# Kernel optimization log

Hardware: AMD Instinct MI355X
Metric: run time of the kernel (lower is better)

The kernel has to match this reference:

```python
import jax, jax.numpy as jnp
import numpy as np

NEG_SLOPE = 0.2
EPS = 1e-16


def _gat_conv(x_src, x_dst, src, dst, W_src, W_dst, a_src, a_dst, b):
    """Single-head bipartite GAT-style conv (gather-score-softmax-scatter)."""
    num_dst = x_dst.shape[0]
    h_src = x_src @ W_src                      # [Ns, C]
    h_dst = x_dst @ W_dst                      # [Nd, C]
    s_src = h_src @ a_src                      # [Ns]
    s_dst = h_dst @ a_dst                      # [Nd]
    e = jax.nn.leaky_relu(s_src[src] + s_dst[dst], NEG_SLOPE)  # [E]
    # segment softmax over incoming edges of each dst node
    m = jax.ops.segment_max(e, dst, num_segments=num_dst)      # [Nd]
    w = jnp.exp(e - m[dst])
    denom = jax.ops.segment_sum(w, dst, num_segments=num_dst)  # [Nd]
    alpha = w / (denom[dst] + EPS)                             # [E]
    out = jax.ops.segment_sum(alpha[:, None] * h_src[src], dst, num_segments=num_dst)
    return out + b


def setup_inputs() -> dict:
    key = jax.random.key(0)
    ks = jax.random.split(key, 32)
    N_a, N_p, N_v = 100000, 150000, 10000
    F_in, C = 768, 64
    E_w, E_c, E_p = 300000, 1500000, 150000
    sc_in = 1.0 / np.sqrt(F_in)
    sc_c = 1.0 / np.sqrt(C)
    inp = {
        'x_author': jax.random.normal(ks[0], (N_a, F_in), jnp.float32),
        'x_paper': jax.random.normal(ks[1], (N_p, F_in), jnp.float32),
        'x_venue': jax.random.normal(ks[2], (N_v, F_in), jnp.float32),
        'writes_src': jax.random.randint(ks[3], (E_w,), 0, N_a, jnp.int32),
        'writes_dst': jax.random.randint(ks[4], (E_w,), 0, N_p, jnp.int32),
        'cites_src': jax.random.randint(ks[5], (E_c,), 0, N_p, jnp.int32),
        'cites_dst': jax.random.randint(ks[6], (E_c,), 0, N_p, jnp.int32),
        'pub_src': jax.random.randint(ks[7], (E_p,), 0, N_v, jnp.int32),
        'pub_dst': jax.random.randint(ks[8], (E_p,), 0, N_p, jnp.int32),
    }
    # per-edge-type learned params: W_src, W_dst [F_in, C], att vecs [C], bias [C]
    names = ['w', 'c', 'p']  # writes, cites, publishes
    for i, n in enumerate(names):
        base = 9 + 5 * i
        inp[f'W{n}_src'] = jax.random.normal(ks[base + 0], (F_in, C), jnp.float32) * sc_in
        inp[f'W{n}_dst'] = jax.random.normal(ks[base + 1], (F_in, C), jnp.float32) * sc_in
        inp[f'a{n}_src'] = jax.random.normal(ks[base + 2], (C,), jnp.float32) * sc_c
        inp[f'a{n}_dst'] = jax.random.normal(ks[base + 3], (C,), jnp.float32) * sc_c
        inp[f'b{n}'] = jnp.zeros((C,), jnp.float32)
    return inp


def reference(x_author, x_paper, x_venue,
              writes_src, writes_dst, cites_src, cites_dst, pub_src, pub_dst,
              Ww_src, Ww_dst, aw_src, aw_dst, bw,
              Wc_src, Wc_dst, ac_src, ac_dst, bc,
              Wp_src, Wp_dst, ap_src, ap_dst, bp):
    # HeteroConv with aggr='sum': all three edge types target 'paper'
    out_w = _gat_conv(x_author, x_paper, writes_src, writes_dst, Ww_src, Ww_dst, aw_src, aw_dst, bw)
    out_c = _gat_conv(x_paper, x_paper, cites_src, cites_dst, Wc_src, Wc_dst, ac_src, ac_dst, bc)
    out_p = _gat_conv(x_venue, x_paper, pub_src, pub_dst, Wp_src, Wp_dst, ap_src, ap_dst, bp)
    return out_w + out_c + out_p  # [N_paper, out_channels]
```

## Files before the change

### kernel.cpp

```cpp
#include <hip/hip_runtime.h>


#define F_IN 768
#define C_OUT 64
#define BN 80
#define TILE_M 64
#define BK 64
#define LDK 72
#define EPS 1e-16f

typedef __bf16 bf16x8 __attribute__((ext_vector_type(8)));
typedef float  f32x4  __attribute__((ext_vector_type(4)));

__global__ void prep_weights(
    const float* __restrict__ Ww_src, const float* __restrict__ aw_src,
    const float* __restrict__ Wc_src, const float* __restrict__ ac_src,
    const float* __restrict__ Wp_src, const float* __restrict__ ap_src,
    const float* __restrict__ Ww_dst, const float* __restrict__ aw_dst,
    const float* __restrict__ Wc_dst, const float* __restrict__ ac_dst,
    const float* __restrict__ Wp_dst, const float* __restrict__ ap_dst,
    __bf16* __restrict__ WTw, __bf16* __restrict__ WTc, __bf16* __restrict__ WTp)
{
    int type = blockIdx.x;
    const float* Ws = (type == 0) ? Ww_src : (type == 1) ? Wc_src : Wp_src;
    const float* as = (type == 0) ? aw_src : (type == 1) ? ac_src : ap_src;
    __bf16* WT = (type == 0) ? WTw : (type == 1) ? WTc : WTp;

    for (int r = threadIdx.x; r < F_IN; r += blockDim.x) {
        const float* wrow = Ws + (size_t)r * C_OUT;
        float u = 0.f;
        for (int c = 0; c < C_OUT; ++c) {
            float wv = wrow[c];
            WT[(size_t)c * F_IN + r] = (__bf16)wv;
            u += wv * as[c];
        }
        WT[(size_t)64 * F_IN + r] = (__bf16)u;
        for (int c = 65; c < BN; ++c) WT[(size_t)c * F_IN + r] = (__bf16)0.f;
        if (type == 1) {
            const float* r1 = Ww_dst + (size_t)r * C_OUT;
            const float* r2 = Wc_dst + (size_t)r * C_OUT;
            const float* r3 = Wp_dst + (size_t)r * C_OUT;
            float vw = 0.f, vc = 0.f, vp = 0.f;
            for (int c = 0; c < C_OUT; ++c) {
                vw += r1[c] * aw_dst[c];
                vc += r2[c] * ac_dst[c];
                vp += r3[c] * ap_dst[c];
            }
            WT[(size_t)65 * F_IN + r] = (__bf16)vw;
            WT[(size_t)66 * F_IN + r] = (__bf16)vc;
            WT[(size_t)67 * F_IN + r] = (__bf16)vp;
        }
    }
}

__global__ __launch_bounds__(256) void gemm_fused(
    const float* __restrict__ X, const __bf16* __restrict__ WT,
    float* __restrict__ H,
    float* __restrict__ s0, float* __restrict__ s1,
    float* __restrict__ s2, float* __restrict__ s3, int M)
{
    __shared__ __bf16 As[TILE_M][LDK];
    __shared__ __bf16 Bs[BN][LDK];

    const int tid  = threadIdx.x;
    const int lane = tid & 63;
    const int warp = tid >> 6;
    const int colq = lane & 15;
    const int quad = lane >> 4;
    const int rowBase = blockIdx.x * TILE_M;

    f32x4 acc[5];
#pragma unroll
    for (int t = 0; t < 5; ++t) acc[t] = (f32x4){0.f, 0.f, 0.f, 0.f};

    const int arow  = tid >> 2;
    const int akoff = (tid & 3) * 16;
    const int grow  = rowBase + arow;
    const bool rowOK = grow < M;
    const float* xrow = X + (size_t)grow * F_IN;

    for (int kc = 0; kc < F_IN; kc += BK) {
        f32x4 av[4];
        if (rowOK) {
            const f32x4* xp = (const f32x4*)(xrow + kc + akoff);
            av[0] = xp[0]; av[1] = xp[1]; av[2] = xp[2]; av[3] = xp[3];
        } else {
#pragma unroll
            for (int i = 0; i < 4; ++i) av[i] = (f32x4){0.f, 0.f, 0.f, 0.f};
        }
        bf16x8 cv[2];
#pragma unroll
        for (int i = 0; i < 4; ++i)
#pragma unroll
            for (int j = 0; j < 4; ++j)
                cv[i >> 1][(i & 1) * 4 + j] = (__bf16)av[i][j];
        *(bf16x8*)&As[arow][akoff]     = cv[0];
        *(bf16x8*)&As[arow][akoff + 8] = cv[1];

        for (int c = tid; c < (BN * BK / 8); c += 256) {
            int br = c >> 3, bo = (c & 7) * 8;
            *(bf16x8*)&Bs[br][bo] =
                *(const bf16x8*)&WT[(size_t)br * F_IN + kc + bo];
        }
        __syncthreads();

#pragma unroll
        for (int kk = 0; kk < BK; kk += 32) {
            bf16x8 a = *(const bf16x8*)&As[warp * 16 + colq][kk + quad * 8];
#pragma unroll
            for (int t = 0; t < 5; ++t) {
                bf16x8 b = *(const bf16x8*)&Bs[t * 16 + colq][kk + quad * 8];
                acc[t] = __builtin_amdgcn_mfma_f32_16x16x32_bf16(a, b, acc[t], 0, 0, 0);
            }
        }
        __syncthreads();
    }

    const int orow0 = rowBase + warp * 16 + quad * 4;
#pragma unroll
    for (int r = 0; r < 4; ++r) {
        int row = orow0 + r;
        if (row < M) {
#pragma unroll
            for (int t = 0; t < 4; ++t)
                H[(size_t)row * C_OUT + t * 16 + colq] = acc[t][r];
            if (colq < 4) {
                float* sp = (colq == 0) ? s0 : (colq == 1) ? s1 : (colq == 2) ? s2 : s3;
                if (sp) sp[row] = acc[4][r];
            }
        }
    }
}

__global__ void hist3(const int* __restrict__ d1, int E1,
                      const int* __restrict__ d2, int E2,
                      const int* __restrict__ d3, int E3,
                      int* __restrict__ cnt)
{
    int i0 = blockIdx.x * blockDim.x + threadIdx.x;
    int stride = gridDim.x * blockDim.x;
    for (int i = i0; i < E1; i += stride) atomicAdd(&cnt[d1[i]], 1);
    for (int i = i0; i < E2; i += stride) atomicAdd(&cnt[d2[i]], 1);
    for (int i = i0; i < E3; i += stride) atomicAdd(&cnt[d3[i]], 1);
}

__global__ void scan1(const int* __restrict__ cnt, int n,
                      int* __restrict__ rowptr, int* __restrict__ bsums)
{
    __shared__ int sm[256];
    const int t = threadIdx.x;
    const int base = blockIdx.x * 1024 + t * 4;
    int v[4];
    int tot = 0;
#pragma unroll
    for (int k = 0; k < 4; ++k) {
        v[k] = (base + k < n) ? cnt[base + k] : 0;
        tot += v[k];
    }
    sm[t] = tot;
    __syncthreads();
    for (int off = 1; off < 256; off <<= 1) {
        int add = (t >= off) ? sm[t - off] : 0;
        __syncthreads();
        sm[t] += add;
        __syncthreads();
    }
    int run = sm[t] - tot;
#pragma unroll
    for (int k = 0; k < 4; ++k) {
        if (base + k < n) rowptr[base + k] = run;
        run += v[k];
    }
    if (t == 255) bsums[blockIdx.x] = sm[255];
}

__global__ void scan2(int* __restrict__ bsums, int nb)
{
    __shared__ int sm[256];
    const int t = threadIdx.x;
    int v = (t < nb) ? bsums[t] : 0;
    sm[t] = v;
    __syncthreads();
    for (int off = 1; off < 256; off <<= 1) {
        int add = (t >= off) ? sm[t - off] : 0;
        __syncthreads();
        sm[t] += add;
        __syncthreads();
    }
    if (t < nb) bsums[t] = sm[t] - v;
}

__global__ void scan3(const int* __restrict__ bsums, int n, int Etot,
                      int* __restrict__ rowptr, int* __restrict__ cursor)
{
    int i = blockIdx.x * blockDim.x + threadIdx.x;
    if (i < n) {
        int r = rowptr[i] + bsums[i >> 10];
        rowptr[i] = r;
        cursor[i] = r;
    }
    if (i == 0) rowptr[n] = Etot;
}

__global__ void edge_sort3(const int* __restrict__ s1, const int* __restrict__ d1, int E1,
                           const int* __restrict__ s2, const int* __restrict__ d2, int E2,
                           const int* __restrict__ s3, const int* __restrict__ d3, int E3,
                           int* __restrict__ cursor, unsigned* __restrict__ eidx)
{
    int i0 = blockIdx.x * blockDim.x + threadIdx.x;
    int stride = gridDim.x * blockDim.x;
    for (int i = i0; i < E1; i += stride) {
        int p = atomicAdd(&cursor[d1[i]], 1);
        eidx[p] = (0u << 24) | (unsigned)s1[i];
    }
    for (int i = i0; i < E2; i += stride) {
        int p = atomicAdd(&cursor[d2[i]], 1);
        eidx[p] = (1u << 24) | (unsigned)s2[i];
    }
    for (int i = i0; i < E3; i += stride) {
        int p = atomicAdd(&cursor[d3[i]], 1);
        eidx[p] = (2u << 24) | (unsigned)s3[i];
    }
}

__global__ __launch_bounds__(256) void gat_gather(
    const unsigned* __restrict__ eidx, const int* __restrict__ rowptr,
    const float* __restrict__ Ha, const float* __restrict__ Hp, const float* __restrict__ Hv,
    const float* __restrict__ ssw, const float* __restrict__ ssc, const float* __restrict__ ssp,
    const float* __restrict__ sdw, const float* __restrict__ sdc, const float* __restrict__ sdp,
    const float* __restrict__ bw, const float* __restrict__ bc, const float* __restrict__ bp,
    float* __restrict__ out, int Nd)
{
    const int lane = threadIdx.x & 63;
    const int q    = lane & 15;
    const int gbase = lane & ~15;
    const int gid  = (blockIdx.x * blockDim.x + threadIdx.x) >> 4;
    const int ng   = (gridDim.x * blockDim.x) >> 4;

    const f32x4* Ha4 = (const f32x4*)Ha;
    const f32x4* Hp4 = (const f32x4*)Hp;
    const f32x4* Hv4 = (const f32x4*)Hv;
    f32x4* out4 = (f32x4*)out;

    const f32x4 b4 = ((const f32x4*)bw)[q] + ((const f32x4*)bc)[q] + ((const f32x4*)bp)[q];

    for (int d = gid; d < Nd; d += ng) {
        const int start = rowptr[d];
        const int end   = rowptr[d + 1];
        const float sd0 = sdw[d], sd1 = sdc[d], sd2 = sdp[d];
        f32x4 a0 = (f32x4){0.f,0.f,0.f,0.f};
        f32x4 a1 = (f32x4){0.f,0.f,0.f,0.f};
        f32x4 a2 = (f32x4){0.f,0.f,0.f,0.f};
        float dn0 = 0.f, dn1 = 0.f, dn2 = 0.f;

        for (int base = start; base < end; base += 16) {
            int n = end - base;
            if (n > 16) n = 16;
            unsigned ew = 0u;
            float w = 0.f;
            if (q < n) {
                ew = eidx[base + q];
                int t = (int)(ew >> 24);
                int s = (int)(ew & 0xFFFFFFu);
                float ss = (t == 0) ? ssw[s] : (t == 1) ? ssc[s] : ssp[s];
                float sd = (t == 0) ? sd0 : (t == 1) ? sd1 : sd2;
                float e = ss + sd;
                e = (e >= 0.f) ? e : 0.2f * e;
                w = __expf(e);
                if (t == 0) dn0 += w; else if (t == 1) dn1 += w; else dn2 += w;
            }
            int j = 0;
            for (; j + 2 <= n; j += 2) {
#pragma unroll
                for (int u = 0; u < 2; ++u) {
                    float wj = __shfl(w, gbase + j + u);
                    unsigned ej = (unsigned)__shfl((int)ew, gbase + j + u);
                    int tj = (int)(ej >> 24);
                    int sj = (int)(ej & 0xFFFFFFu);
                    const f32x4* Hr = (tj == 0) ? Ha4 : (tj == 1) ? Hp4 : Hv4;
                    f32x4 hv = Hr[(size_t)sj * 16 + q];
                    if (tj == 0) a0 += wj * hv;
                    else if (tj == 1) a1 += wj * hv;
                    else a2 += wj * hv;
                }
            }
            for (; j < n; ++j) {
                float wj = __shfl(w, gbase + j);
                unsigned ej = (unsigned)__shfl((int)ew, gbase + j);
                int tj = (int)(ej >> 24);
                int sj = (int)(ej & 0xFFFFFFu);
                const f32x4* Hr = (tj == 0) ? Ha4 : (tj == 1) ? Hp4 : Hv4;
                f32x4 hv = Hr[(size_t)sj * 16 + q];
                if (tj == 0) a0 += wj * hv;
                else if (tj == 1) a1 += wj * hv;
                else a2 += wj * hv;
            }
        }
#pragma unroll
        for (int off = 8; off > 0; off >>= 1) {
            dn0 += __shfl_xor(dn0, off);
            dn1 += __shfl_xor(dn1, off);
            dn2 += __shfl_xor(dn2, off);
        }
        f32x4 res = a0 / (dn0 + EPS) + a1 / (dn1 + EPS) + a2 / (dn2 + EPS) + b4;
        out4[(size_t)d * 16 + q] = res;
    }
}

extern "C" void kernel_launch(void* const* d_in, const int* in_sizes, int n_in,
                              void* d_out, int out_size, void* d_ws, size_t ws_size,
                              hipStream_t stream)
{
    const float* x_a = (const float*)d_in[0];
    const float* x_p = (const float*)d_in[1];
    const float* x_v = (const float*)d_in[2];
    const int* w_src = (const int*)d_in[3];
    const int* w_dst = (const int*)d_in[4];
    const int* c_src = (const int*)d_in[5];
    const int* c_dst = (const int*)d_in[6];
    const int* p_src = (const int*)d_in[7];
    const int* p_dst = (const int*)d_in[8];
    const float* Ww_src = (const float*)d_in[9];
    const float* Ww_dst = (const float*)d_in[10];
    const float* aw_src = (const float*)d_in[11];
    const float* aw_dst = (const float*)d_in[12];
    const float* bw     = (const float*)d_in[13];
    const float* Wc_src = (const float*)d_in[14];
    const float* Wc_dst = (const float*)d_in[15];
    const float* ac_src = (const float*)d_in[16];
    const float* ac_dst = (const float*)d_in[17];
    const float* bc     = (const float*)d_in[18];
    const float* Wp_src = (const float*)d_in[19];
    const float* Wp_dst = (const float*)d_in[20];
    const float* ap_src = (const float*)d_in[21];
    const float* ap_dst = (const float*)d_in[22];
    const float* bp     = (const float*)d_in[23];
    float* out = (float*)d_out;

    const int Na = in_sizes[0] / F_IN;
    const int Np = in_sizes[1] / F_IN;
    const int Nv = in_sizes[2] / F_IN;
    const int Ew = in_sizes[3];
    const int Ec = in_sizes[5];
    const int Ep = in_sizes[7];
    const int Etot = Ew + Ec + Ep;

    char* ws = (char*)d_ws;
    size_t off = 0;
    auto alloc = [&](size_t bytes) -> void* {
        off = (off + 255) & ~(size_t)255;
        void* p = ws + off;
        off += bytes;
        return p;
    };
    __bf16* WTw = (__bf16*)alloc((size_t)BN * F_IN * 2);
    __bf16* WTc = (__bf16*)alloc((size_t)BN * F_IN * 2);
    __bf16* WTp = (__bf16*)alloc((size_t)BN * F_IN * 2);
    float* Ha = (float*)alloc((size_t)Na * C_OUT * 4);
    float* Hp = (float*)alloc((size_t)Np * C_OUT * 4);
    float* Hv = (float*)alloc((size_t)Nv * C_OUT * 4);
    float* s_w_src = (float*)alloc((size_t)Na * 4);
    float* s_c_src = (float*)alloc((size_t)Np * 4);
    float* s_p_src = (float*)alloc((size_t)Nv * 4);
    float* s_w_dst = (float*)alloc((size_t)Np * 4);
    float* s_c_dst = (float*)alloc((size_t)Np * 4);
    float* s_p_dst = (float*)alloc((size_t)Np * 4);
    int* cnt    = (int*)alloc((size_t)Np * 4);
    int* rowptr = (int*)alloc((size_t)(Np + 1) * 4);
    int* cursor = (int*)alloc((size_t)Np * 4);
    int* bsums  = (int*)alloc(1024);
    unsigned* eidx = (unsigned*)alloc((size_t)Etot * 4);
    (void)ws_size; (void)n_in; (void)out_size;

    hipMemsetAsync(cnt, 0, (size_t)Np * 4, stream);

    prep_weights<<<3, 256, 0, stream>>>(
        Ww_src, aw_src, Wc_src, ac_src, Wp_src, ap_src,
        Ww_dst, aw_dst, Wc_dst, ac_dst, Wp_dst, ap_dst,
        WTw, WTc, WTp);

    gemm_fused<<<(Na + TILE_M - 1) / TILE_M, 256, 0, stream>>>(
        x_a, WTw, Ha, s_w_src, nullptr, nullptr, nullptr, Na);
    gemm_fused<<<(Np + TILE_M - 1) / TILE_M, 256, 0, stream>>>(
        x_p, WTc, Hp, s_c_src, s_w_dst, s_c_dst, s_p_dst, Np);
    gemm_fused<<<(Nv + TILE_M - 1) / TILE_M, 256, 0, stream>>>(
        x_v, WTp, Hv, s_p_src, nullptr, nullptr, nullptr, Nv);

    hist3<<<1024, 256, 0, stream>>>(w_dst, Ew, c_dst, Ec, p_dst, Ep, cnt);
    const int NB = (Np + 1023) / 1024;
    scan1<<<NB, 256, 0, stream>>>(cnt, Np, rowptr, bsums);
    scan2<<<1, 256, 0, stream>>>(bsums, NB);
    scan3<<<(Np + 255) / 256, 256, 0, stream>>>(bsums, Np, Etot, rowptr, cursor);
    edge_sort3<<<1024, 256, 0, stream>>>(
        w_src, w_dst, Ew, c_src, c_dst, Ec, p_src, p_dst, Ep, cursor, eidx);

    gat_gather<<<2048, 256, 0, stream>>>(
        eidx, rowptr, Ha, Hp, Hv,
        s_w_src, s_c_src, s_p_src, s_w_dst, s_c_dst, s_p_dst,
        bw, bc, bp, out, Np);
}
```

Baseline: 1.282 ms.

## Merge GEMMs with edge sort, split CSR by edge type, drop LDS staging

The weight prep and histogram now run in one launch, and the three projection GEMMs and the edge bucketing run in a second merged launch, so independent work shares the GPU. The CSR is split into three segments per destination, one per edge type. This removes the type tag and the per-edge branching in the gather, which now calls a simpler segment-sum helper. The GEMM drops shared-memory staging and reads X and the bf16 weights directly into registers, with a software prefetch of the next K chunk. The trade-offs are a three-times larger count, scan and rowptr array, scans that handle 2048 elements per block, and weight reads that rely on cache instead of LDS reuse.

```diff
diff --git a/kernel.cpp b/kernel.cpp
--- a/kernel.cpp
+++ b/kernel.cpp
@@ -6,142 +6,62 @@
 #define BN 80
 #define TILE_M 64
 #define BK 64
-#define LDK 72
 #define EPS 1e-16f
 
 typedef __bf16 bf16x8 __attribute__((ext_vector_type(8)));
 typedef float  f32x4  __attribute__((ext_vector_type(4)));
 
-__global__ void prep_weights(
+__global__ void prep_hist(
     const float* __restrict__ Ww_src, const float* __restrict__ aw_src,
     const float* __restrict__ Wc_src, const float* __restrict__ ac_src,
     const float* __restrict__ Wp_src, const float* __restrict__ ap_src,
     const float* __restrict__ Ww_dst, const float* __restrict__ aw_dst,
     const float* __restrict__ Wc_dst, const float* __restrict__ ac_dst,
     const float* __restrict__ Wp_dst, const float* __restrict__ ap_dst,
-    __bf16* __restrict__ WTw, __bf16* __restrict__ WTc, __bf16* __restrict__ WTp)
-{
-    int type = blockIdx.x;
-    const float* Ws = (type == 0) ? Ww_src : (type == 1) ? Wc_src : Wp_src;
-    const float* as = (type == 0) ? aw_src : (type == 1) ? ac_src : ap_src;
-    __bf16* WT = (type == 0) ? WTw : (type == 1) ? WTc : WTp;
-
-    for (int r = threadIdx.x; r < F_IN; r += blockDim.x) {
-        const float* wrow = Ws + (size_t)r * C_OUT;
-        float u = 0.f;
-        for (int c = 0; c < C_OUT; ++c) {
-            float wv = wrow[c];
-            WT[(size_t)c * F_IN + r] = (__bf16)wv;
-            u += wv * as[c];
-        }
-        WT[(size_t)64 * F_IN + r] = (__bf16)u;
-        for (int c = 65; c < BN; ++c) WT[(size_t)c * F_IN + r] = (__bf16)0.f;
-        if (type == 1) {
-            const float* r1 = Ww_dst + (size_t)r * C_OUT;
-            const float* r2 = Wc_dst + (size_t)r * C_OUT;
-            const float* r3 = Wp_dst + (size_t)r * C_OUT;
-            float vw = 0.f, vc = 0.f, vp = 0.f;
+    __bf16* __restrict__ WTw, __bf16* __restrict__ WTc, __bf16* __restrict__ WTp,
+    const int* __restrict__ d1, int E1,
+    const int* __restrict__ d2, int E2,
+    const int* __restrict__ d3, int E3,
+    int* __restrict__ cnt)
+{
+    if (blockIdx.x < 3) {
+        int type = blockIdx.x;
+        const float* Ws = (type == 0) ? Ww_src : (type == 1) ? Wc_src : Wp_src;
+        const float* as = (type == 0) ? aw_src : (type == 1) ? ac_src : ap_src;
+        __bf16* WT = (type == 0) ? WTw : (type == 1) ? WTc : WTp;
+
+        for (int r = threadIdx.x; r < F_IN; r += blockDim.x) {
+            const float* wrow = Ws + (size_t)r * C_OUT;
+            float u = 0.f;
             for (int c = 0; c < C_OUT; ++c) {
-                vw += r1[c] * aw_dst[c];
-                vc += r2[c] * ac_dst[c];
-                vp += r3[c] * ap_dst[c];
+                float wv = wrow[c];
+                WT[(size_t)c * F_IN + r] = (__bf16)wv;
+                u += wv * as[c];
             }
-            WT[(size_t)65 * F_IN + r] = (__bf16)vw;
-            WT[(size_t)66 * F_IN + r] = (__bf16)vc;
-            WT[(size_t)67 * F_IN + r] = (__bf16)vp;
-        }
-    }
-}
-
-__global__ __launch_bounds__(256) void gemm_fused(
-    const float* __restrict__ X, const __bf16* __restrict__ WT,
-    float* __restrict__ H,
-    float* __restrict__ s0, float* __restrict__ s1,
-    float* __restrict__ s2, float* __restrict__ s3, int M)
-{
-    __shared__ __bf16 As[TILE_M][LDK];
-    __shared__ __bf16 Bs[BN][LDK];
-
-    const int tid  = threadIdx.x;
-    const int lane = tid & 63;
-    const int warp = tid >> 6;
-    const int colq = lane & 15;
-    const int quad = lane >> 4;
-    const int rowBase = blockIdx.x * TILE_M;
-
-    f32x4 acc[5];
-#pragma unroll
-    for (int t = 0; t < 5; ++t) acc[t] = (f32x4){0.f, 0.f, 0.f, 0.f};
-
-    const int arow  = tid >> 2;
-    const int akoff = (tid & 3) * 16;
-    const int grow  = rowBase + arow;
-    const bool rowOK = grow < M;
-    const float* xrow = X + (size_t)grow * F_IN;
-
-    for (int kc = 0; kc < F_IN; kc += BK) {
-        f32x4 av[4];
-        if (rowOK) {
-            const f32x4* xp = (const f32x4*)(xrow + kc + akoff);
-            av[0] = xp[0]; av[1] = xp[1]; av[2] = xp[2]; av[3] = xp[3];
-        } else {
-#pragma unroll
-            for (int i = 0; i < 4; ++i) av[i] = (f32x4){0.f, 0.f, 0.f, 0.f};
-        }
-        bf16x8 cv[2];
-#pragma unroll
-        for (int i = 0; i < 4; ++i)
-#pragma unroll
-            for (int j = 0; j < 4; ++j)
-                cv[i >> 1][(i & 1) * 4 + j] = (__bf16)av[i][j];
-        *(bf16x8*)&As[arow][akoff]     = cv[0];
-        *(bf16x8*)&As[arow][akoff + 8] = cv[1];
-
-        for (int c = tid; c < (BN * BK / 8); c += 256) {
-            int br = c >> 3, bo = (c & 7) * 8;
-            *(bf16x8*)&Bs[br][bo] =
-                *(const bf16x8*)&WT[(size_t)br * F_IN + kc + bo];
-        }
-        __syncthreads();
-
-#pragma unroll
-        for (int kk = 0; kk < BK; kk += 32) {
-            bf16x8 a = *(const bf16x8*)&As[warp * 16 + colq][kk + quad * 8];
-#pragma unroll
-            for (int t = 0; t < 5; ++t) {
-                bf16x8 b = *(const bf16x8*)&Bs[t * 16 + colq][kk + quad * 8];
-                acc[t] = __builtin_amdgcn_mfma_f32_16x16x32_bf16(a, b, acc[t], 0, 0, 0);
+            WT[(size_t)64 * F_IN + r] = (__bf16)u;
+            for (int c = 65; c < BN; ++c) WT[(size_t)c * F_IN + r] = (__bf16)0.f;
+            if (type == 1) {
+                const float* r1 = Ww_dst + (size_t)r * C_OUT;
+                const float* r2 = Wc_dst + (size_t)r * C_OUT;
+                const float* r3 = Wp_dst + (size_t)r * C_OUT;
+                float vw = 0.f, vc = 0.f, vp = 0.f;
+                for (int c = 0; c < C_OUT; ++c) {
+                    vw += r1[c] * aw_dst[c];
+                    vc += r2[c] * ac_dst[c];
+                    vp += r3[c] * ap_dst[c];
+                }
+                WT[(size_t)65 * F_IN + r] = (__bf16)vw;
+                WT[(size_t)66 * F_IN + r] = (__bf16)vc;
+                WT[(size_t)67 * F_IN + r] = (__bf16)vp;
             }
         }
-        __syncthreads();
-    }
-
-    const int orow0 = rowBase + warp * 16 + quad * 4;
-#pragma unroll
-    for (int r = 0; r < 4; ++r) {
-        int row = orow0 + r;
-        if (row < M) {
-#pragma unroll
-            for (int t = 0; t < 4; ++t)
-                H[(size_t)row * C_OUT + t * 16 + colq] = acc[t][r];
-            if (colq < 4) {
-                float* sp = (colq == 0) ? s0 : (colq == 1) ? s1 : (colq == 2) ? s2 : s3;
-                if (sp) sp[row] = acc[4][r];
-            }
-        }
-    }
-}
-
-__global__ void hist3(const int* __restrict__ d1, int E1,
-                      const int* __restrict__ d2, int E2,
-                      const int* __restrict__ d3, int E3,
-                      int* __restrict__ cnt)
-{
-    int i0 = blockIdx.x * blockDim.x + threadIdx.x;
-    int stride = gridDim.x * blockDim.x;
-    for (int i = i0; i < E1; i += stride) atomicAdd(&cnt[d1[i]], 1);
-    for (int i = i0; i < E2; i += stride) atomicAdd(&cnt[d2[i]], 1);
-    for (int i = i0; i < E3; i += stride) atomicAdd(&cnt[d3[i]], 1);
+        return;
+    }
+    int i0 = (blockIdx.x - 3) * blockDim.x + threadIdx.x;
+    int stride = (gridDim.x - 3) * blockDim.x;
+    for (int i = i0; i < E1; i += stride) atomicAdd(&cnt[3 * d1[i] + 0], 1);
+    for (int i = i0; i < E2; i += stride) atomicAdd(&cnt[3 * d2[i] + 1], 1);
+    for (int i = i0; i < E3; i += stride) atomicAdd(&cnt[3 * d3[i] + 2], 1);
 }
 
 __global__ void scan1(const int* __restrict__ cnt, int n,
@@ -149,11 +69,11 @@
 {
     __shared__ int sm[256];
     const int t = threadIdx.x;
-    const int base = blockIdx.x * 1024 + t * 4;
-    int v[4];
+    const int base = blockIdx.x * 2048 + t * 8;
+    int v[8];
     int tot = 0;
 #pragma unroll
-    for (int k = 0; k < 4; ++k) {
+    for (int k = 0; k < 8; ++k) {
         v[k] = (base + k < n) ? cnt[base + k] : 0;
         tot += v[k];
     }
@@ -167,7 +87,7 @@
     }
     int run = sm[t] - tot;
 #pragma unroll
-    for (int k = 0; k < 4; ++k) {
+    for (int k = 0; k < 8; ++k) {
         if (base + k < n) rowptr[base + k] = run;
         run += v[k];
     }
@@ -195,32 +115,158 @@
 {
     int i = blockIdx.x * blockDim.x + threadIdx.x;
     if (i < n) {
-        int r = rowptr[i] + bsums[i >> 10];
+        int r = rowptr[i] + bsums[i >> 11];
         rowptr[i] = r;
         cursor[i] = r;
     }
     if (i == 0) rowptr[n] = Etot;
 }
 
-__global__ void edge_sort3(const int* __restrict__ s1, const int* __restrict__ d1, int E1,
-                           const int* __restrict__ s2, const int* __restrict__ d2, int E2,
-                           const int* __restrict__ s3, const int* __restrict__ d3, int E3,
-                           int* __restrict__ cursor, unsigned* __restrict__ eidx)
-{
-    int i0 = blockIdx.x * blockDim.x + threadIdx.x;
-    int stride = gridDim.x * blockDim.x;
-    for (int i = i0; i < E1; i += stride) {
-        int p = atomicAdd(&cursor[d1[i]], 1);
-        eidx[p] = (0u << 24) | (unsigned)s1[i];
-    }
-    for (int i = i0; i < E2; i += stride) {
-        int p = atomicAdd(&cursor[d2[i]], 1);
-        eidx[p] = (1u << 24) | (unsigned)s2[i];
-    }
-    for (int i = i0; i < E3; i += stride) {
-        int p = atomicAdd(&cursor[d3[i]], 1);
-        eidx[p] = (2u << 24) | (unsigned)s3[i];
-    }
+__global__ __launch_bounds__(256) void gemm_sort(
+    const float* __restrict__ xa, const float* __restrict__ xp, const float* __restrict__ xv,
+    const __bf16* __restrict__ WTw, const __bf16* __restrict__ WTc, const __bf16* __restrict__ WTp,
+    float* __restrict__ Ha, float* __restrict__ Hp, float* __restrict__ Hv,
+    float* __restrict__ ssw, float* __restrict__ ssc, float* __restrict__ ssp,
+    float* __restrict__ sdw, float* __restrict__ sdc, float* __restrict__ sdp,
+    int Na, int Np, int Nv, int BA, int BP, int BV,
+    const int* __restrict__ ws_, const int* __restrict__ wd_, int Ew,
+    const int* __restrict__ cs_, const int* __restrict__ cd_, int Ec,
+    const int* __restrict__ ps_, const int* __restrict__ pd_, int Ep,
+    int* __restrict__ cursor, unsigned* __restrict__ eidx)
+{
+    const int bid = blockIdx.x;
+    const int tid = threadIdx.x;
+    const int NG = BA + BP + BV;
+
+    if (bid >= NG) {
+        int i0 = (bid - NG) * blockDim.x + tid;
+        int stride = (gridDim.x - NG) * blockDim.x;
+        for (int i = i0; i < Ew; i += stride) {
+            int p = atomicAdd(&cursor[3 * wd_[i] + 0], 1);
+            eidx[p] = (unsigned)ws_[i];
+        }
+        for (int i = i0; i < Ec; i += stride) {
+            int p = atomicAdd(&cursor[3 * cd_[i] + 1], 1);
+            eidx[p] = (unsigned)cs_[i];
+        }
+        for (int i = i0; i < Ep; i += stride) {
+            int p = atomicAdd(&cursor[3 * pd_[i] + 2], 1);
+            eidx[p] = (unsigned)ps_[i];
+        }
+        return;
+    }
+
+    const float* X; const __bf16* WT; float* H;
+    float *s0, *s1, *s2, *s3; int M, rb;
+    if (bid < BA)           { X = xa; WT = WTw; H = Ha; s0 = ssw; s1 = s2 = s3 = nullptr; M = Na; rb = bid; }
+    else if (bid < BA + BP) { X = xp; WT = WTc; H = Hp; s0 = ssc; s1 = sdw; s2 = sdc; s3 = sdp; M = Np; rb = bid - BA; }
+    else                    { X = xv; WT = WTp; H = Hv; s0 = ssp; s1 = s2 = s3 = nullptr; M = Nv; rb = bid - BA - BP; }
+
+    const int lane = tid & 63;
+    const int warp = tid >> 6;
+    const int colq = lane & 15;
+    const int quad = lane >> 4;
+    const int rowBase = rb * TILE_M;
+    const int grow = rowBase + warp * 16 + colq;
+    const bool rowOK = grow < M;
+    const float* xrow = X + (size_t)grow * F_IN + quad * 8;
+    const __bf16* wrow = WT + (size_t)colq * F_IN + quad * 8;
+
+    f32x4 acc[5];
+#pragma unroll
+    for (int t = 0; t < 5; ++t) acc[t] = (f32x4){0.f, 0.f, 0.f, 0.f};
+
+    f32x4 x0{}, x1{}, x2{}, x3{};
+    if (rowOK) {
+        x0 = *(const f32x4*)(xrow);
+        x1 = *(const f32x4*)(xrow + 4);
+        x2 = *(const f32x4*)(xrow + 32);
+        x3 = *(const f32x4*)(xrow + 36);
+    }
+
+    for (int ci = 0; ci < F_IN / BK; ++ci) {
+        const int kc = ci * BK;
+        f32x4 n0{}, n1{}, n2{}, n3{};
+        if (rowOK && ci + 1 < F_IN / BK) {
+            const float* xn = xrow + kc + BK;
+            n0 = *(const f32x4*)(xn);
+            n1 = *(const f32x4*)(xn + 4);
+            n2 = *(const f32x4*)(xn + 32);
+            n3 = *(const f32x4*)(xn + 36);
+        }
+        bf16x8 av0, av1;
+#pragma unroll
+        for (int j = 0; j < 4; ++j) {
+            av0[j] = (__bf16)x0[j]; av0[4 + j] = (__bf16)x1[j];
+            av1[j] = (__bf16)x2[j]; av1[4 + j] = (__bf16)x3[j];
+        }
+        const __bf16* wp = wrow + kc;
+#pragma unroll
+        for (int t = 0; t < 5; ++t) {
+            bf16x8 b = *(const bf16x8*)(wp + (size_t)t * 16 * F_IN);
+            acc[t] = __builtin_amdgcn_mfma_f32_16x16x32_bf16(av0, b, acc[t], 0, 0, 0);
+        }
+#pragma unroll
+        for (int t = 0; t < 5; ++t) {
+            bf16x8 b = *(const bf16x8*)(wp + (size_t)t * 16 * F_IN + 32);
+            acc[t] = __builtin_amdgcn_mfma_f32_16x16x32_bf16(av1, b, acc[t], 0, 0, 0);
+        }
+        x0 = n0; x1 = n1; x2 = n2; x3 = n3;
+    }
+
+    const int orow0 = rowBase + warp * 16 + quad * 4;
+#pragma unroll
+    for (int r = 0; r < 4; ++r) {
+        int row = orow0 + r;
+        if (row < M) {
+#pragma unroll
+            for (int t = 0; t < 4; ++t)
+                H[(size_t)row * C_OUT + t * 16 + colq] = acc[t][r];
+            if (colq < 4) {
+                float* sp = (colq == 0) ? s0 : (colq == 1) ? s1 : (colq == 2) ? s2 : s3;
+                if (sp) sp[row] = acc[4][r];
+            }
+        }
+    }
+}
+
+static __device__ __forceinline__ f32x4 segsum(
+    const unsigned* __restrict__ eidx, int beg, int end,
+    const float* __restrict__ ss, float sd,
+    const f32x4* __restrict__ H4, int q, int gbase)
+{
+    f32x4 at = (f32x4){0.f, 0.f, 0.f, 0.f};
+    float dn = 0.f;
+    for (int base = beg; base < end; base += 16) {
+        int n = end - base;
+        if (n > 16) n = 16;
+        float w = 0.f;
+        int s = 0;
+        if (q < n) {
+            s = (int)eidx[base + q];
+            float e = ss[s] + sd;
+            e = (e >= 0.f) ? e : 0.2f * e;
+            w = __expf(e);
+            dn += w;
+        }
+        int j = 0;
+        for (; j + 4 <= n; j += 4) {
+#pragma unroll
+            for (int u = 0; u < 4; ++u) {
+                float wj = __shfl(w, gbase + j + u);
+                int sj = __shfl(s, gbase + j + u);
+                at += wj * H4[(size_t)sj * 16 + q];
+            }
+        }
+        for (; j < n; ++j) {
+            float wj = __shfl(w, gbase + j);
+            int sj = __shfl(s, gbase + j);
+            at += wj * H4[(size_t)sj * 16 + q];
+        }
+    }
+#pragma unroll
+    for (int off = 8; off > 0; off >>= 1) dn += __shfl_xor(dn, off);
+    return at / (dn + EPS);
 }
 
 __global__ __launch_bounds__(256) void gat_gather(
@@ -245,64 +291,14 @@
     const f32x4 b4 = ((const f32x4*)bw)[q] + ((const f32x4*)bc)[q] + ((const f32x4*)bp)[q];
 
     for (int d = gid; d < Nd; d += ng) {
-        const int start = rowptr[d];
-        const int end   = rowptr[d + 1];
-        const float sd0 = sdw[d], sd1 = sdc[d], sd2 = sdp[d];
-        f32x4 a0 = (f32x4){0.f,0.f,0.f,0.f};
-        f32x4 a1 = (f32x4){0.f,0.f,0.f,0.f};
-        f32x4 a2 = (f32x4){0.f,0.f,0.f,0.f};
-        float dn0 = 0.f, dn1 = 0.f, dn2 = 0.f;
-
-        for (int base = start; base < end; base += 16) {
-            int n = end - base;
-            if (n > 16) n = 16;
-            unsigned ew = 0u;
-            float w = 0.f;
-            if (q < n) {
-                ew = eidx[base + q];
-                int t = (int)(ew >> 24);
-                int s = (int)(ew & 0xFFFFFFu);
-                float ss = (t == 0) ? ssw[s] : (t == 1) ? ssc[s] : ssp[s];
-                float sd = (t == 0) ? sd0 : (t == 1) ? sd1 : sd2;
-                float e = ss + sd;
-                e = (e >= 0.f) ? e : 0.2f * e;
-                w = __expf(e);
-                if (t == 0) dn0 += w; else if (t == 1) dn1 += w; else dn2 += w;
-            }
-            int j = 0;
-            for (; j + 2 <= n; j += 2) {
-#pragma unroll
-                for (int u = 0; u < 2; ++u) {
-                    float wj = __shfl(w, gbase + j + u);
-                    unsigned ej = (unsigned)__shfl((int)ew, gbase + j + u);
-                    int tj = (int)(ej >> 24);
-                    int sj = (int)(ej & 0xFFFFFFu);
-                    const f32x4* Hr = (tj == 0) ? Ha4 : (tj == 1) ? Hp4 : Hv4;
-                    f32x4 hv = Hr[(size_t)sj * 16 + q];
-                    if (tj == 0) a0 += wj * hv;
-                    else if (tj == 1) a1 += wj * hv;
-                    else a2 += wj * hv;
-                }
-            }
-            for (; j < n; ++j) {
-                float wj = __shfl(w, gbase + j);
-                unsigned ej = (unsigned)__shfl((int)ew, gbase + j);
-                int tj = (int)(ej >> 24);
-                int sj = (int)(ej & 0xFFFFFFu);
-                const f32x4* Hr = (tj == 0) ? Ha4 : (tj == 1) ? Hp4 : Hv4;
-                f32x4 hv = Hr[(size_t)sj * 16 + q];
-                if (tj == 0) a0 += wj * hv;
-                else if (tj == 1) a1 += wj * hv;
-                else a2 += wj * hv;
-            }
-        }
-#pragma unroll
-        for (int off = 8; off > 0; off >>= 1) {
-            dn0 += __shfl_xor(dn0, off);
-            dn1 += __shfl_xor(dn1, off);
-            dn2 += __shfl_xor(dn2, off);
-        }
-        f32x4 res = a0 / (dn0 + EPS) + a1 / (dn1 + EPS) + a2 / (dn2 + EPS) + b4;
+        const int r0 = rowptr[3 * d];
+        const int r1 = rowptr[3 * d + 1];
+        const int r2 = rowptr[3 * d + 2];
+        const int r3 = rowptr[3 * d + 3];
+        f32x4 res = b4;
+        res += segsum(eidx, r0, r1, ssw, sdw[d], Ha4, q, gbase);
+        res += segsum(eidx, r1, r2, ssc, sdc[d], Hp4, q, gbase);
+        res += segsum(eidx, r2, r3, ssp, sdp[d], Hv4, q, gbase);
         out4[(size_t)d * 16 + q] = res;
     }
 }
@@ -344,6 +340,7 @@
     const int Ec = in_sizes[5];
     const int Ep = in_sizes[7];
     const int Etot = Ew + Ec + Ep;
+    const int NSEG = 3 * Np;
 
     char* ws = (char*)d_ws;
     size_t off = 0;
@@ -365,34 +362,35 @@
     float* s_w_dst = (float*)alloc((size_t)Np * 4);
     float* s_c_dst = (float*)alloc((size_t)Np * 4);
     float* s_p_dst = (float*)alloc((size_t)Np * 4);
-    int* cnt    = (int*)alloc((size_t)Np * 4);
-    int* rowptr = (int*)alloc((size_t)(Np + 1) * 4);
-    int* cursor = (int*)alloc((size_t)Np * 4);
+    int* cnt    = (int*)alloc((size_t)NSEG * 4);
+    int* rowptr = (int*)alloc((size_t)(NSEG + 1) * 4);
+    int* cursor = (int*)alloc((size_t)NSEG * 4);
     int* bsums  = (int*)alloc(1024);
     unsigned* eidx = (unsigned*)alloc((size_t)Etot * 4);
     (void)ws_size; (void)n_in; (void)out_size;
 
-    hipMemsetAsync(cnt, 0, (size_t)Np * 4, stream);
-
-    prep_weights<<<3, 256, 0, stream>>>(
+    hipMemsetAsync(cnt, 0, (size_t)NSEG * 4, stream);
+
+    prep_hist<<<3 + 1024, 256, 0, stream>>>(
         Ww_src, aw_src, Wc_src, ac_src, Wp_src, ap_src,
         Ww_dst, aw_dst, Wc_dst, ac_dst, Wp_dst, ap_dst,
-        WTw, WTc, WTp);
-
-    gemm_fused<<<(Na + TILE_M - 1) / TILE_M, 256, 0, stream>>>(
-        x_a, WTw, Ha, s_w_src, nullptr, nullptr, nullptr, Na);
-    gemm_fused<<<(Np + TILE_M - 1) / TILE_M, 256, 0, stream>>>(
-        x_p, WTc, Hp, s_c_src, s_w_dst, s_c_dst, s_p_dst, Np);
-    gemm_fused<<<(Nv + TILE_M - 1) / TILE_M, 256, 0, stream>>>(
-        x_v, WTp, Hv, s_p_src, nullptr, nullptr, nullptr, Nv);
-
-    hist3<<<1024, 256, 0, stream>>>(w_dst, Ew, c_dst, Ec, p_dst, Ep, cnt);
-    const int NB = (Np + 1023) / 1024;
-    scan1<<<NB, 256, 0, stream>>>(cnt, Np, rowptr, bsums);
+        WTw, WTc, WTp,
+        w_dst, Ew, c_dst, Ec, p_dst, Ep, cnt);
+
+    const int NB = (NSEG + 2047) / 2048;
+    scan1<<<NB, 256, 0, stream>>>(cnt, NSEG, rowptr, bsums);
     scan2<<<1, 256, 0, stream>>>(bsums, NB);
-    scan3<<<(Np + 255) / 256, 256, 0, stream>>>(bsums, Np, Etot, rowptr, cursor);
-    edge_sort3<<<1024, 256, 0, stream>>>(
-        w_src, w_dst, Ew, c_src, c_dst, Ec, p_src, p_dst, Ep, cursor, eidx);
+    scan3<<<(NSEG + 255) / 256, 256, 0, stream>>>(bsums, NSEG, Etot, rowptr, cursor);
+
+    const int BA = (Na + TILE_M - 1) / TILE_M;
+    const int BP = (Np + TILE_M - 1) / TILE_M;
+    const int BV = (Nv + TILE_M - 1) / TILE_M;
+    gemm_sort<<<BA + BP + BV + 1024, 256, 0, stream>>>(
+        x_a, x_p, x_v, WTw, WTc, WTp, Ha, Hp, Hv,
+        s_w_src, s_c_src, s_p_src, s_w_dst, s_c_dst, s_p_dst,
+        Na, Np, Nv, BA, BP, BV,
+        w_src, w_dst, Ew, c_src, c_dst, Ec, p_src, p_dst, Ep,
+        cursor, eidx);
 
     gat_gather<<<2048, 256, 0, stream>>>(
         eidx, rowptr, Ha, Hp, Hv,
```

After: 1.277 ms. No clear change (-0.4%).
